# Kernel optimization log

Hardware: AMD Instinct MI355X
Metric: run time of the kernel (lower is better)

Reference implementation:

```python
import jax, jax.numpy as jnp
import numpy as np

K, N = 8192, 8192
GROUP_SIZE = 128
N_GROUPS = N // GROUP_SIZE  # 64
NBITS = 4
B, T = 8, 32


def setup_inputs() -> dict:
    key = jax.random.key(0)
    k_x, k_q, k_s, k_z, k_m1, k_m2, k_b = jax.random.split(key, 7)
    x = jax.random.normal(k_x, (B, T, N), dtype=jnp.float32)
    # int8 quantized weight codes in [0, 2**nbits - 1]
    W_q = jax.random.randint(k_q, (K, N), 0, 2 ** NBITS, dtype=jnp.int32)
    # group-wise scales/zeros, shaped for broadcast against [K, n_groups, group_size]
    scales = jax.random.uniform(k_s, (K, N_GROUPS, 1), dtype=jnp.float32, minval=0.01, maxval=0.1)
    zeros = jax.random.uniform(k_z, (K, N_GROUPS, 1), dtype=jnp.float32, minval=0.0, maxval=2.0 ** NBITS - 1.0)
    # Sinkhorn row/col scaling factors (positive, near 1)
    mu1 = jnp.exp(0.1 * jax.random.normal(k_m1, (N,), dtype=jnp.float32))
    mu2 = jnp.exp(0.1 * jax.random.normal(k_m2, (K,), dtype=jnp.float32))
    bias = jax.random.normal(k_b, (K,), dtype=jnp.float32)
    return {"x": x, "W_q": W_q, "scales": scales, "zeros": zeros,
            "mu1": mu1, "mu2": mu2, "bias": bias}


def reference(x, W_q, scales, zeros, mu1, mu2, bias):
    k, n = W_q.shape
    n_groups = scales.shape[1]
    group_size = n // n_groups
    # group-wise dequant: (Q - zero) * scale, then Sinkhorn row/col rescale
    Q_g = W_q.astype(jnp.float32).reshape(k, n_groups, group_size)
    W_deq = ((Q_g - zeros) * scales).reshape(k, n)
    W_deq = W_deq * mu2[:, None] * mu1[None, :]
    W_deq = W_deq.astype(x.dtype)
    # nn.functional.linear: x @ W^T + b ; x: [B, T, N] -> [B, T, K]
    out = jnp.einsum('btn,kn->btk', x, W_deq) + bias
    return out
```

## Files before the change

kernel.cpp:

```cpp
#include <hip/hip_runtime.h>
#include <hip/hip_bf16.h>

#define M_DIM 256
#define K_DIM 8192
#define N_DIM 8192
#define NGRP  64

#define BN 128
#define BK 32
#define THREADS 512
#define SPLITN 8
#define CHUNK  (N_DIM / SPLITN)
#define NSTEPS (CHUNK / BK)
#define NG     (CHUNK >> 7)

#define ASIZE 16384
#define BSIZE 8192
#define B_OFF  (3 * ASIZE)
#define SL_OFF (B_OFF + 2 * BSIZE)
#define LDS_TOTAL (SL_OFF + NG * 128 * 8)

typedef __bf16 bf16x8 __attribute__((ext_vector_type(8)));
typedef __bf16 bf16x4 __attribute__((ext_vector_type(4)));
typedef float  f32x4  __attribute__((ext_vector_type(4)));

#define SW(a) ((a) ^ ((((a) >> 7) & 7) << 4))

#define GLOAD_LDS16(g, l) __builtin_amdgcn_global_load_lds( \
    (const __attribute__((address_space(1))) void*)(g),     \
    (__attribute__((address_space(3))) void*)(l), 16, 0, 0)

__global__ __launch_bounds__(256) void prep_xs(const float* __restrict__ x,
                                               const float* __restrict__ mu1,
                                               __bf16* __restrict__ xs) {
    int t  = blockIdx.x * 256 + threadIdx.x;
    int n4 = t & 2047;
    int m  = t >> 11;
    int n  = n4 << 2;
    float4 xv = *(const float4*)(x + (size_t)m * N_DIM + n);
    float4 mv = *(const float4*)(mu1 + n);
    bf16x4 o;
    o[0] = (__bf16)(xv.x * mv.x);
    o[1] = (__bf16)(xv.y * mv.y);
    o[2] = (__bf16)(xv.z * mv.z);
    o[3] = (__bf16)(xv.w * mv.w);
    *(bf16x4*)(xs + (size_t)m * N_DIM + n) = o;
}

__global__ __launch_bounds__(THREADS, 4)
void gemm_q(const __bf16* __restrict__ xs, const int* __restrict__ Wq,
            const float* __restrict__ scales, const float* __restrict__ zeros,
            __bf16* __restrict__ partial) {
    extern __shared__ __align__(1024) char lds[];

    const int b     = blockIdx.x;
    const int split = b & 7;
    const int kidx  = b >> 3;
    const int k0    = kidx * BN;
    const int nbase = split * CHUNK;
    const int gbase = split * NG;

    const int tid  = threadIdx.x;
    const int lane = tid & 63;
    const int w    = tid >> 6;
    const int wm   = w >> 2;
    const int wn   = w & 3;
    const int start = kidx & (NSTEPS - 1);

    float* SL = (float*)(lds + SL_OFF);

    {
        int r = tid >> 2, gq = tid & 3;
#pragma unroll
        for (int gg = 0; gg < (NG >> 2); ++gg) {
            int g = (gg << 2) | gq;
            size_t si = (size_t)(k0 + r) * NGRP + gbase + g;
            float s = scales[si];
            float z = zeros[si];
            float2 v; v.x = s; v.y = -z * s;
            *(float2*)&SL[(size_t)((g << 7) + r) * 2] = v;
        }
    }
    asm volatile("s_waitcnt vmcnt(0) lgkmcnt(0)" ::: "memory");
    __builtin_amdgcn_s_barrier();

    const char* asrc[2];
    int aoff[2];
#pragma unroll
    for (int cc = 0; cc < 2; ++cc) {
        int c   = w * 2 + cc;
        int off = c * 1024 + lane * 16;
        int L   = SW(off);
        aoff[cc] = off;
        asrc[cc] = (const char*)xs + ((size_t)(L >> 6) * N_DIM) * 2 + (L & 63);
    }

    const int brow = w * 16 + (lane >> 2);
    const int bq   = lane & 3;
    const int* bptr0 = Wq + (size_t)(k0 + brow) * N_DIM + bq * 8;
    char* bdst0 = lds + B_OFF + SW(brow * 64 + bq * 16);

    const int rboff0 = SW((wn * 32 + 0  + (lane & 15)) * 64 + (lane >> 4) * 16);
    const int rboff1 = SW((wn * 32 + 16 + (lane & 15)) * 64 + (lane >> 4) * 16);

    char* pA0 = lds;
    char* pA1 = lds + ASIZE;
    char* pA2 = lds + 2 * ASIZE;

#define ISSUE_A(t, pbuf)                                                  \
    {                                                                     \
        int s_ = ((t) + start) & (NSTEPS - 1);                            \
        size_t so_ = (size_t)(nbase + s_ * BK) * 2;                       \
        GLOAD_LDS16(asrc[0] + so_, (pbuf) + aoff[0]);                     \
        GLOAD_LDS16(asrc[1] + so_, (pbuf) + aoff[1]);                     \
    }
#define LOAD_B(t, q0, q1)                                                 \
    {                                                                     \
        int s_ = ((t) + start) & (NSTEPS - 1);                            \
        const int* p_ = bptr0 + (nbase + s_ * BK);                        \
        q0 = *(const int4*)p_;                                            \
        q1 = *(const int4*)(p_ + 4);                                      \
    }

    f32x4 acc[8][2];
#pragma unroll
    for (int i = 0; i < 8; ++i) {
        acc[i][0] = (f32x4){0.f, 0.f, 0.f, 0.f};
        acc[i][1] = (f32x4){0.f, 0.f, 0.f, 0.f};
    }

    int4 qa0, qa1, qb0, qb1;

    LOAD_B(0, qa0, qa1);
    asm volatile("" ::: "memory");
    ISSUE_A(0, pA0);
    asm volatile("" ::: "memory");
    LOAD_B(1, qb0, qb1);

#define STEP(it, q0c, q1c, W1, W4, DO_A, DO_B)                            \
    {                                                                     \
        asm volatile("s_waitcnt vmcnt(" #W1 ")" ::: "memory");            \
        int scur_ = ((it) + start) & (NSTEPS - 1);                        \
        float2 sz_ = *(float2*)&SL[(size_t)(((scur_ >> 2) << 7) + brow) * 2]; \
        bf16x8 wv_;                                                       \
        wv_[0] = (__bf16)((float)q0c.x * sz_.x + sz_.y);                  \
        wv_[1] = (__bf16)((float)q0c.y * sz_.x + sz_.y);                  \
        wv_[2] = (__bf16)((float)q0c.z * sz_.x + sz_.y);                  \
        wv_[3] = (__bf16)((float)q0c.w * sz_.x + sz_.y);                  \
        wv_[4] = (__bf16)((float)q1c.x * sz_.x + sz_.y);                  \
        wv_[5] = (__bf16)((float)q1c.y * sz_.x + sz_.y);                  \
        wv_[6] = (__bf16)((float)q1c.z * sz_.x + sz_.y);                  \
        wv_[7] = (__bf16)((float)q1c.w * sz_.x + sz_.y);                  \
        *(bf16x8*)(bdst0 + ((it) & 1) * BSIZE) = wv_;                     \
        if (DO_A) { ISSUE_A((it) + 1, pA1); }                             \
        asm volatile("" ::: "memory");                                    \
        if (DO_B) { LOAD_B((it) + 2, q0c, q1c); }                         \
        asm volatile("s_waitcnt vmcnt(" #W4 ") lgkmcnt(0)" ::: "memory"); \
        __builtin_amdgcn_s_barrier();                                     \
        const char* bufA_ = pA0;                                          \
        const char* bufB_ = lds + B_OFF + ((it) & 1) * BSIZE;             \
        bf16x8 bv0_ = *(const bf16x8*)(bufB_ + rboff0);                   \
        bf16x8 bv1_ = *(const bf16x8*)(bufB_ + rboff1);                   \
        __builtin_amdgcn_s_setprio(1);                                    \
        _Pragma("unroll")                                                 \
        for (int mi = 0; mi < 8; ++mi) {                                  \
            int la_ = (wm * 128 + mi * 16 + (lane & 15)) * 64 + (lane >> 4) * 16; \
            bf16x8 av_ = *(const bf16x8*)(bufA_ + SW(la_));               \
            acc[mi][0] = __builtin_amdgcn_mfma_f32_16x16x32_bf16(av_, bv0_, acc[mi][0], 0, 0, 0); \
            acc[mi][1] = __builtin_amdgcn_mfma_f32_16x16x32_bf16(av_, bv1_, acc[mi][1], 0, 0, 0); \
        }                                                                 \
        __builtin_amdgcn_s_setprio(0);                                    \
        { char* t_ = pA0; pA0 = pA1; pA1 = pA2; pA2 = t_; }               \
    }

    for (int it = 0; it < NSTEPS - 2; it += 2) {
        STEP(it,     qa0, qa1, 4, 6, true, true);
        STEP(it + 1, qb0, qb1, 4, 6, true, true);
    }
    STEP(NSTEPS - 2, qa0, qa1, 4, 4, true,  false);
    STEP(NSTEPS - 1, qb0, qb1, 2, 0, false, false);
#undef STEP
#undef ISSUE_A
#undef LOAD_B

    __bf16* outp = partial + (size_t)split * ((size_t)M_DIM * K_DIM);
#pragma unroll
    for (int mi = 0; mi < 8; ++mi) {
#pragma unroll
        for (int ci = 0; ci < 2; ++ci) {
            int gk = k0 + wn * 32 + ci * 16 + (lane & 15);
            int gm = wm * 128 + mi * 16 + (lane >> 4) * 4;
#pragma unroll
            for (int rix = 0; rix < 4; ++rix)
                outp[(size_t)(gm + rix) * K_DIM + gk] = (__bf16)acc[mi][ci][rix];
        }
    }
}

__global__ __launch_bounds__(256) void reduce_out(const __bf16* __restrict__ partial,
                                                  const float* __restrict__ mu2,
                                                  const float* __restrict__ bias,
                                                  float* __restrict__ out) {
    int t  = blockIdx.x * 256 + threadIdx.x;
    int k4 = t & 2047;
    int m  = t >> 11;
    size_t base = (size_t)m * K_DIM + (size_t)k4 * 4;
    float4 s; s.x = 0.f; s.y = 0.f; s.z = 0.f; s.w = 0.f;
#pragma unroll
    for (int sp = 0; sp < SPLITN; ++sp) {
        bf16x4 p = *(const bf16x4*)(partial + (size_t)sp * ((size_t)M_DIM * K_DIM) + base);
        s.x += (float)p[0]; s.y += (float)p[1]; s.z += (float)p[2]; s.w += (float)p[3];
    }
    float4 m2 = *(const float4*)(mu2 + (size_t)k4 * 4);
    float4 bi = *(const float4*)(bias + (size_t)k4 * 4);
    float4 o;
    o.x = s.x * m2.x + bi.x;
    o.y = s.y * m2.y + bi.y;
    o.z = s.z * m2.z + bi.z;
    o.w = s.w * m2.w + bi.w;
    *(float4*)(out + base) = o;
}

extern "C" void kernel_launch(void* const* d_in, const int* in_sizes, int n_in,
                              void* d_out, int out_size, void* d_ws, size_t ws_size,
                              hipStream_t stream) {
    const float* x      = (const float*)d_in[0];
    const int*   Wq     = (const int*)d_in[1];
    const float* scales = (const float*)d_in[2];
    const float* zeros  = (const float*)d_in[3];
    const float* mu1    = (const float*)d_in[4];
    const float* mu2    = (const float*)d_in[5];
    const float* bias   = (const float*)d_in[6];
    float* out = (float*)d_out;

    __bf16* xs = (__bf16*)d_ws;
    const size_t xs_bytes = (size_t)M_DIM * N_DIM * sizeof(__bf16);
    __bf16* partial = (__bf16*)((char*)d_ws + xs_bytes);

    (void)hipFuncSetAttribute((const void*)gemm_q,
                              hipFuncAttributeMaxDynamicSharedMemorySize,
                              LDS_TOTAL);

    prep_xs<<<2048, 256, 0, stream>>>(x, mu1, xs);
    gemm_q<<<64 * SPLITN, THREADS, LDS_TOTAL, stream>>>(xs, Wq, scales, zeros, partial);
    reduce_out<<<2048, 256, 0, stream>>>(partial, mu2, bias, out);
}
```

Baseline: 89.50 us.

## Repack int32 weight codes into packed 4-bit words before GEMM

Adds a repack kernel that packs each group of eight int32 weight codes into one 32-bit word of 4-bit nibbles. The GEMM then loads one dword per thread per step instead of two int4 vectors, and unpacks the nibbles with shifts and masks; the vmcnt wait counts are adjusted to match. The aim is to shrink the weight traffic inside the GEMM main loop. The repack runs on every call, though, and still reads the full int32 weight matrix and writes the packed copy, so total memory traffic and launch count go up.

```diff
diff --git a/kernel.cpp b/kernel.cpp
--- a/kernel.cpp
+++ b/kernel.cpp
@@ -5,6 +5,7 @@
 #define K_DIM 8192
 #define N_DIM 8192
 #define NGRP  64
+#define NW    (N_DIM / 8)
 
 #define BN 128
 #define BK 32
@@ -29,6 +30,22 @@
 #define GLOAD_LDS16(g, l) __builtin_amdgcn_global_load_lds( \
     (const __attribute__((address_space(1))) void*)(g),     \
     (__attribute__((address_space(3))) void*)(l), 16, 0, 0)
+
+__global__ __launch_bounds__(256) void repack_w4(const int* __restrict__ Wq,
+                                                 unsigned* __restrict__ Wq4) {
+    const int total = (K_DIM * N_DIM) / 8;
+    int t = blockIdx.x * 256 + threadIdx.x;
+    for (int i = t; i < total; i += 256 * 2048) {
+        const int* p = Wq + (size_t)i * 8;
+        int4 a = *(const int4*)p;
+        int4 b = *(const int4*)(p + 4);
+        unsigned wv =  (unsigned)(a.x & 15)        | ((unsigned)(a.y & 15) << 4)
+                    | ((unsigned)(a.z & 15) << 8)  | ((unsigned)(a.w & 15) << 12)
+                    | ((unsigned)(b.x & 15) << 16) | ((unsigned)(b.y & 15) << 20)
+                    | ((unsigned)(b.z & 15) << 24) | ((unsigned)(b.w & 15) << 28);
+        Wq4[i] = wv;
+    }
+}
 
 __global__ __launch_bounds__(256) void prep_xs(const float* __restrict__ x,
                                                const float* __restrict__ mu1,
@@ -48,7 +65,7 @@
 }
 
 __global__ __launch_bounds__(THREADS, 4)
-void gemm_q(const __bf16* __restrict__ xs, const int* __restrict__ Wq,
+void gemm_q(const __bf16* __restrict__ xs, const unsigned* __restrict__ Wq4,
             const float* __restrict__ scales, const float* __restrict__ zeros,
             __bf16* __restrict__ partial) {
     extern __shared__ __align__(1024) char lds[];
@@ -97,7 +114,7 @@
 
     const int brow = w * 16 + (lane >> 2);
     const int bq   = lane & 3;
-    const int* bptr0 = Wq + (size_t)(k0 + brow) * N_DIM + bq * 8;
+    const unsigned* bptr0 = Wq4 + (size_t)(k0 + brow) * NW + (nbase >> 3) + bq;
     char* bdst0 = lds + B_OFF + SW(brow * 64 + bq * 16);
 
     const int rboff0 = SW((wn * 32 + 0  + (lane & 15)) * 64 + (lane >> 4) * 16);
@@ -114,12 +131,10 @@
         GLOAD_LDS16(asrc[0] + so_, (pbuf) + aoff[0]);                     \
         GLOAD_LDS16(asrc[1] + so_, (pbuf) + aoff[1]);                     \
     }
-#define LOAD_B(t, q0, q1)                                                 \
+#define LOAD_B(t, q)                                                      \
     {                                                                     \
         int s_ = ((t) + start) & (NSTEPS - 1);                            \
-        const int* p_ = bptr0 + (nbase + s_ * BK);                        \
-        q0 = *(const int4*)p_;                                            \
-        q1 = *(const int4*)(p_ + 4);                                      \
+        q = bptr0[s_ * (BK / 8)];                                         \
     }
 
     f32x4 acc[8][2];
@@ -129,32 +144,33 @@
         acc[i][1] = (f32x4){0.f, 0.f, 0.f, 0.f};
     }
 
-    int4 qa0, qa1, qb0, qb1;
-
-    LOAD_B(0, qa0, qa1);
+    unsigned qa, qb;
+
+    LOAD_B(0, qa);
     asm volatile("" ::: "memory");
     ISSUE_A(0, pA0);
     asm volatile("" ::: "memory");
-    LOAD_B(1, qb0, qb1);
-
-#define STEP(it, q0c, q1c, W1, W4, DO_A, DO_B)                            \
+    LOAD_B(1, qb);
+
+#define STEP(it, q, W1, W4, DO_A, DO_B)                                   \
     {                                                                     \
         asm volatile("s_waitcnt vmcnt(" #W1 ")" ::: "memory");            \
         int scur_ = ((it) + start) & (NSTEPS - 1);                        \
         float2 sz_ = *(float2*)&SL[(size_t)(((scur_ >> 2) << 7) + brow) * 2]; \
+        unsigned qw_ = q;                                                 \
         bf16x8 wv_;                                                       \
-        wv_[0] = (__bf16)((float)q0c.x * sz_.x + sz_.y);                  \
-        wv_[1] = (__bf16)((float)q0c.y * sz_.x + sz_.y);                  \
-        wv_[2] = (__bf16)((float)q0c.z * sz_.x + sz_.y);                  \
-        wv_[3] = (__bf16)((float)q0c.w * sz_.x + sz_.y);                  \
-        wv_[4] = (__bf16)((float)q1c.x * sz_.x + sz_.y);                  \
-        wv_[5] = (__bf16)((float)q1c.y * sz_.x + sz_.y);                  \
-        wv_[6] = (__bf16)((float)q1c.z * sz_.x + sz_.y);                  \
-        wv_[7] = (__bf16)((float)q1c.w * sz_.x + sz_.y);                  \
+        wv_[0] = (__bf16)((float)( qw_        & 15u) * sz_.x + sz_.y);    \
+        wv_[1] = (__bf16)((float)((qw_ >> 4)  & 15u) * sz_.x + sz_.y);    \
+        wv_[2] = (__bf16)((float)((qw_ >> 8)  & 15u) * sz_.x + sz_.y);    \
+        wv_[3] = (__bf16)((float)((qw_ >> 12) & 15u) * sz_.x + sz_.y);    \
+        wv_[4] = (__bf16)((float)((qw_ >> 16) & 15u) * sz_.x + sz_.y);    \
+        wv_[5] = (__bf16)((float)((qw_ >> 20) & 15u) * sz_.x + sz_.y);    \
+        wv_[6] = (__bf16)((float)((qw_ >> 24) & 15u) * sz_.x + sz_.y);    \
+        wv_[7] = (__bf16)((float)( qw_ >> 28       ) * sz_.x + sz_.y);    \
         *(bf16x8*)(bdst0 + ((it) & 1) * BSIZE) = wv_;                     \
         if (DO_A) { ISSUE_A((it) + 1, pA1); }                             \
         asm volatile("" ::: "memory");                                    \
-        if (DO_B) { LOAD_B((it) + 2, q0c, q1c); }                         \
+        if (DO_B) { LOAD_B((it) + 2, q); }                                \
         asm volatile("s_waitcnt vmcnt(" #W4 ") lgkmcnt(0)" ::: "memory"); \
         __builtin_amdgcn_s_barrier();                                     \
         const char* bufA_ = pA0;                                          \
@@ -174,11 +190,11 @@
     }
 
     for (int it = 0; it < NSTEPS - 2; it += 2) {
-        STEP(it,     qa0, qa1, 4, 6, true, true);
-        STEP(it + 1, qb0, qb1, 4, 6, true, true);
-    }
-    STEP(NSTEPS - 2, qa0, qa1, 4, 4, true,  false);
-    STEP(NSTEPS - 1, qb0, qb1, 2, 0, false, false);
+        STEP(it,     qa, 3, 4, true, true);
+        STEP(it + 1, qb, 3, 4, true, true);
+    }
+    STEP(NSTEPS - 2, qa, 3, 3, true,  false);
+    STEP(NSTEPS - 1, qb, 2, 0, false, false);
 #undef STEP
 #undef ISSUE_A
 #undef LOAD_B
@@ -236,12 +252,15 @@
     __bf16* xs = (__bf16*)d_ws;
     const size_t xs_bytes = (size_t)M_DIM * N_DIM * sizeof(__bf16);
     __bf16* partial = (__bf16*)((char*)d_ws + xs_bytes);
+    const size_t part_bytes = (size_t)SPLITN * M_DIM * K_DIM * sizeof(__bf16);
+    unsigned* Wq4 = (unsigned*)((char*)d_ws + xs_bytes + part_bytes);
 
     (void)hipFuncSetAttribute((const void*)gemm_q,
                               hipFuncAttributeMaxDynamicSharedMemorySize,
                               LDS_TOTAL);
 
+    repack_w4<<<2048, 256, 0, stream>>>(Wq, Wq4);
     prep_xs<<<2048, 256, 0, stream>>>(x, mu1, xs);
-    gemm_q<<<64 * SPLITN, THREADS, LDS_TOTAL, stream>>>(xs, Wq, scales, zeros, partial);
+    gemm_q<<<64 * SPLITN, THREADS, LDS_TOTAL, stream>>>(xs, Wq4, scales, zeros, partial);
     reduce_out<<<2048, 256, 0, stream>>>(partial, mu2, bias, out);
 }
```

Measured after the change: 123.3 us. +37.7%, slower.

## Reshape warp tiling to 64x64 and prefetch A tiles two steps ahead

Applied to the files above, without the earlier changes.

Warps are rearranged from a 2x4 grid of 128x32 tiles to a 4x2 grid of 64x64 tiles. Each step now does 4 A reads plus 4 B reads from LDS instead of 8 A reads plus 2 B reads, which cuts shared-memory read traffic per MFMA. The A global-to-LDS prefetch moves to two steps ahead, issued after the barrier through the triple buffer, and the per-step vmcnt waits are simplified. The risk is that this reordered wait/issue schedule is tight against the triple-buffer reuse, and B register reads now go through an indexed array.

```diff
diff --git a/kernel.cpp b/kernel.cpp
--- a/kernel.cpp
+++ b/kernel.cpp
@@ -63,8 +63,8 @@
     const int tid  = threadIdx.x;
     const int lane = tid & 63;
     const int w    = tid >> 6;
-    const int wm   = w >> 2;
-    const int wn   = w & 3;
+    const int wmq  = w >> 1;
+    const int wnh  = w & 1;
     const int start = kidx & (NSTEPS - 1);
 
     float* SL = (float*)(lds + SL_OFF);
@@ -100,8 +100,12 @@
     const int* bptr0 = Wq + (size_t)(k0 + brow) * N_DIM + bq * 8;
     char* bdst0 = lds + B_OFF + SW(brow * 64 + bq * 16);
 
-    const int rboff0 = SW((wn * 32 + 0  + (lane & 15)) * 64 + (lane >> 4) * 16);
-    const int rboff1 = SW((wn * 32 + 16 + (lane & 15)) * 64 + (lane >> 4) * 16);
+    int rb[4], ra[4];
+#pragma unroll
+    for (int i = 0; i < 4; ++i) {
+        rb[i] = SW((wnh * 64 + i * 16 + (lane & 15)) * 64 + (lane >> 4) * 16);
+        ra[i] = SW((wmq * 64 + i * 16 + (lane & 15)) * 64 + (lane >> 4) * 16);
+    }
 
     char* pA0 = lds;
     char* pA1 = lds + ASIZE;
@@ -122,12 +126,12 @@
         q1 = *(const int4*)(p_ + 4);                                      \
     }
 
-    f32x4 acc[8][2];
-#pragma unroll
-    for (int i = 0; i < 8; ++i) {
-        acc[i][0] = (f32x4){0.f, 0.f, 0.f, 0.f};
-        acc[i][1] = (f32x4){0.f, 0.f, 0.f, 0.f};
-    }
+    f32x4 acc[4][4];
+#pragma unroll
+    for (int i = 0; i < 4; ++i)
+#pragma unroll
+        for (int j = 0; j < 4; ++j)
+            acc[i][j] = (f32x4){0.f, 0.f, 0.f, 0.f};
 
     int4 qa0, qa1, qb0, qb1;
 
@@ -136,10 +140,12 @@
     ISSUE_A(0, pA0);
     asm volatile("" ::: "memory");
     LOAD_B(1, qb0, qb1);
-
-#define STEP(it, q0c, q1c, W1, W4, DO_A, DO_B)                            \
+    asm volatile("" ::: "memory");
+    ISSUE_A(1, pA1);
+
+#define STEP(it, q0c, q1c, W1N, DO_ISS)                                   \
     {                                                                     \
-        asm volatile("s_waitcnt vmcnt(" #W1 ")" ::: "memory");            \
+        asm volatile("s_waitcnt vmcnt(" #W1N ")" ::: "memory");           \
         int scur_ = ((it) + start) & (NSTEPS - 1);                        \
         float2 sz_ = *(float2*)&SL[(size_t)(((scur_ >> 2) << 7) + brow) * 2]; \
         bf16x8 wv_;                                                       \
@@ -152,44 +158,45 @@
         wv_[6] = (__bf16)((float)q1c.z * sz_.x + sz_.y);                  \
         wv_[7] = (__bf16)((float)q1c.w * sz_.x + sz_.y);                  \
         *(bf16x8*)(bdst0 + ((it) & 1) * BSIZE) = wv_;                     \
-        if (DO_A) { ISSUE_A((it) + 1, pA1); }                             \
-        asm volatile("" ::: "memory");                                    \
-        if (DO_B) { LOAD_B((it) + 2, q0c, q1c); }                         \
-        asm volatile("s_waitcnt vmcnt(" #W4 ") lgkmcnt(0)" ::: "memory"); \
+        if (DO_ISS) { LOAD_B((it) + 2, q0c, q1c); }                       \
+        asm volatile("s_waitcnt lgkmcnt(0)" ::: "memory");                \
         __builtin_amdgcn_s_barrier();                                     \
-        const char* bufA_ = pA0;                                          \
         const char* bufB_ = lds + B_OFF + ((it) & 1) * BSIZE;             \
-        bf16x8 bv0_ = *(const bf16x8*)(bufB_ + rboff0);                   \
-        bf16x8 bv1_ = *(const bf16x8*)(bufB_ + rboff1);                   \
+        bf16x8 bv0_ = *(const bf16x8*)(bufB_ + rb[0]);                    \
+        bf16x8 bv1_ = *(const bf16x8*)(bufB_ + rb[1]);                    \
+        bf16x8 bv2_ = *(const bf16x8*)(bufB_ + rb[2]);                    \
+        bf16x8 bv3_ = *(const bf16x8*)(bufB_ + rb[3]);                    \
+        if (DO_ISS) { ISSUE_A((it) + 2, pA2); }                           \
         __builtin_amdgcn_s_setprio(1);                                    \
         _Pragma("unroll")                                                 \
-        for (int mi = 0; mi < 8; ++mi) {                                  \
-            int la_ = (wm * 128 + mi * 16 + (lane & 15)) * 64 + (lane >> 4) * 16; \
-            bf16x8 av_ = *(const bf16x8*)(bufA_ + SW(la_));               \
+        for (int mi = 0; mi < 4; ++mi) {                                  \
+            bf16x8 av_ = *(const bf16x8*)(pA0 + ra[mi]);                  \
             acc[mi][0] = __builtin_amdgcn_mfma_f32_16x16x32_bf16(av_, bv0_, acc[mi][0], 0, 0, 0); \
             acc[mi][1] = __builtin_amdgcn_mfma_f32_16x16x32_bf16(av_, bv1_, acc[mi][1], 0, 0, 0); \
+            acc[mi][2] = __builtin_amdgcn_mfma_f32_16x16x32_bf16(av_, bv2_, acc[mi][2], 0, 0, 0); \
+            acc[mi][3] = __builtin_amdgcn_mfma_f32_16x16x32_bf16(av_, bv3_, acc[mi][3], 0, 0, 0); \
         }                                                                 \
         __builtin_amdgcn_s_setprio(0);                                    \
         { char* t_ = pA0; pA0 = pA1; pA1 = pA2; pA2 = t_; }               \
     }
 
     for (int it = 0; it < NSTEPS - 2; it += 2) {
-        STEP(it,     qa0, qa1, 4, 6, true, true);
-        STEP(it + 1, qb0, qb1, 4, 6, true, true);
-    }
-    STEP(NSTEPS - 2, qa0, qa1, 4, 4, true,  false);
-    STEP(NSTEPS - 1, qb0, qb1, 2, 0, false, false);
+        STEP(it,     qa0, qa1, 4, true);
+        STEP(it + 1, qb0, qb1, 4, true);
+    }
+    STEP(NSTEPS - 2, qa0, qa1, 4, false);
+    STEP(NSTEPS - 1, qb0, qb1, 0, false);
 #undef STEP
 #undef ISSUE_A
 #undef LOAD_B
 
     __bf16* outp = partial + (size_t)split * ((size_t)M_DIM * K_DIM);
 #pragma unroll
-    for (int mi = 0; mi < 8; ++mi) {
-#pragma unroll
-        for (int ci = 0; ci < 2; ++ci) {
-            int gk = k0 + wn * 32 + ci * 16 + (lane & 15);
-            int gm = wm * 128 + mi * 16 + (lane >> 4) * 4;
+    for (int mi = 0; mi < 4; ++mi) {
+#pragma unroll
+        for (int ci = 0; ci < 4; ++ci) {
+            int gk = k0 + wnh * 64 + ci * 16 + (lane & 15);
+            int gm = wmq * 64 + mi * 16 + (lane >> 4) * 4;
 #pragma unroll
             for (int rix = 0; rix < 4; ++rix)
                 outp[(size_t)(gm + rix) * K_DIM + gk] = (__bf16)acc[mi][ci][rix];
```

Result: faster. 84.67 us (median of 2 runs) (-5.4%).
